# Performance work log

Hardware: AMD Instinct MI355X
Metric: run time of the kernel (lower is better)

The kernel has to match this reference:

```python
import jax, jax.numpy as jnp
import numpy as np

N = 100000      # nodes
E = 1200000     # edges (avg degree 12)
DIN = 64        # input_dim
HID = 64        # hidden_dim
HEADS = 4
CH = HID // 4   # 16 per-head channels; concat -> HID


def setup_inputs() -> dict:
    key = jax.random.key(0)
    ks = jax.random.split(key, 16)
    s = 0.05
    return {
        "x": jax.random.normal(ks[0], (N, DIN), jnp.float32),
        "edge_index": jax.random.randint(ks[1], (2, E), 0, N, jnp.int32),
        # GCN layers
        "W1": s * jax.random.normal(ks[2], (DIN, HID), jnp.float32),
        "b1": jnp.zeros((HID,), jnp.float32),
        "W2": s * jax.random.normal(ks[3], (HID, HID), jnp.float32),
        "b2": jnp.zeros((HID,), jnp.float32),
        "W3": s * jax.random.normal(ks[4], (HID, HID // 2), jnp.float32),
        "b3": jnp.zeros((HID // 2,), jnp.float32),
        # GAT layer: in = HID//2 = 32, out per head = HID//4 = 16, 4 heads concat -> 64
        "Wg": s * jax.random.normal(ks[5], (HID // 2, HEADS * CH), jnp.float32),
        "att_src": s * jax.random.normal(ks[6], (HEADS, CH), jnp.float32),
        "att_dst": s * jax.random.normal(ks[7], (HEADS, CH), jnp.float32),
        "bg": jnp.zeros((HEADS * CH,), jnp.float32),
        # classifier MLP
        "Wc1": s * jax.random.normal(ks[8], (HID, HID // 2), jnp.float32),
        "bc1": jnp.zeros((HID // 2,), jnp.float32),
        "Wc2": s * jax.random.normal(ks[9], (HID // 2, 2), jnp.float32),
        "bc2": jnp.zeros((2,), jnp.float32),
    }


def reference(x, edge_index, W1, b1, W2, b2, W3, b3,
              Wg, att_src, att_dst, bg, Wc1, bc1, Wc2, bc2):
    n = x.shape[0]
    # add self-loops (PyG default for GCNConv and GATConv)
    loops = jnp.arange(n, dtype=edge_index.dtype)
    src = jnp.concatenate([edge_index[0], loops])
    dst = jnp.concatenate([edge_index[1], loops])

    # symmetric GCN normalization: deg^-1/2[src] * deg^-1/2[dst]
    deg = jax.ops.segment_sum(jnp.ones(src.shape, x.dtype), dst, num_segments=n)
    dinv = jnp.where(deg > 0, jax.lax.rsqrt(deg), 0.0)
    norm = (dinv[src] * dinv[dst])[:, None]  # [E+N, 1]

    def gcn(h, W, b):
        h = h @ W                                   # [N, out]
        msg = h[src] * norm                         # gather + scale, [E+N, out]
        return jax.ops.segment_sum(msg, dst, num_segments=n) + b

    h = jax.nn.relu(gcn(x, W1, b1))   # dropout = identity (eval mode)
    h = jax.nn.relu(gcn(h, W2, b2))
    h = jax.nn.relu(gcn(h, W3, b3))   # [N, HID//2]

    # GATConv, 4 heads, concat
    heads, ch = att_src.shape
    g = (h @ Wg).reshape(n, heads, ch)                       # [N, H, C]
    a_s = jnp.einsum('nhc,hc->nh', g, att_src)               # [N, H]
    a_d = jnp.einsum('nhc,hc->nh', g, att_dst)
    e = jax.nn.leaky_relu(a_s[src] + a_d[dst], 0.2)          # [E+N, H]
    m = jax.ops.segment_max(e, dst, num_segments=n)          # per-dst max
    ex = jnp.exp(e - m[dst])
    den = jax.ops.segment_sum(ex, dst, num_segments=n)
    alpha = ex / den[dst]                                    # segment softmax
    o = jax.ops.segment_sum(g[src] * alpha[:, :, None], dst, num_segments=n)
    o = jax.nn.relu(o.reshape(n, heads * ch) + bg)           # [N, HID]

    pooled = jnp.mean(o, axis=0, keepdims=True)              # batch=None path: [1, HID]
    z = jax.nn.relu(pooled @ Wc1 + bc1)
    return z @ Wc2 + bc2                                     # [1, 2]
```

## Files before the change

kernel.cpp:

```cpp
#include <hip/hip_runtime.h>
#include <hip/hip_bf16.h>
#include <hip/hip_fp16.h>
#include <math.h>

__device__ __forceinline__ unsigned h2u(__half2 h) { return *reinterpret_cast<unsigned*>(&h); }
__device__ __forceinline__ __half2 u2h(unsigned u) { return *reinterpret_cast<__half2*>(&u); }
__device__ __forceinline__ __half2 shfl_h2(__half2 h, int off) {
  int v = __shfl_xor((int)h2u(h), off);
  unsigned uv = (unsigned)v;
  return u2h(uv);
}


#define P1E 16
#define NBK 400

__global__ __launch_bounds__(256) void bucket_hist(const int* __restrict__ dst,
                                                   int* __restrict__ bcnt, int e) {
  __shared__ int lcnt[NBK];
  for (int i = threadIdx.x; i < NBK; i += 256) lcnt[i] = 0;
  __syncthreads();
  int base = blockIdx.x * (256 * P1E);
#pragma unroll
  for (int r = 0; r < P1E; ++r) {
    int i = base + r * 256 + threadIdx.x;
    if (i < e) atomicAdd(&lcnt[dst[i] >> 8], 1);
  }
  __syncthreads();
  for (int b = threadIdx.x; b < NBK; b += 256)
    if (lcnt[b]) atomicAdd(&bcnt[b], lcnt[b]);
}

__global__ __launch_bounds__(512) void bucket_scan(const int* __restrict__ bcnt,
                                                   int* __restrict__ bucket_base,
                                                   int* __restrict__ gcursor,
                                                   int nb, int e) {
  __shared__ int s[512];
  int v = (threadIdx.x < (unsigned)nb) ? bcnt[threadIdx.x] : 0;
  s[threadIdx.x] = v;
  __syncthreads();
  for (int off = 1; off < 512; off <<= 1) {
    int t = (threadIdx.x >= (unsigned)off) ? s[threadIdx.x - off] : 0;
    __syncthreads();
    s[threadIdx.x] += t;
    __syncthreads();
  }
  if (threadIdx.x < (unsigned)nb) {
    int excl = s[threadIdx.x] - v;
    bucket_base[threadIdx.x] = excl;
    gcursor[threadIdx.x] = excl;
  }
  if (threadIdx.x == 0) bucket_base[nb] = e;
}

__global__ __launch_bounds__(256) void bin_pass1(const int* __restrict__ src,
                                                 const int* __restrict__ dst,
                                                 int* __restrict__ gcursor,
                                                 unsigned* __restrict__ stream, int e) {
  __shared__ int lcnt[NBK], gbase[NBK];
  for (int i = threadIdx.x; i < NBK; i += 256) lcnt[i] = 0;
  __syncthreads();
  int base = blockIdx.x * (256 * P1E);
  int rankr[P1E];
#pragma unroll
  for (int r = 0; r < P1E; ++r) {
    int i = base + r * 256 + threadIdx.x;
    rankr[r] = (i < e) ? atomicAdd(&lcnt[dst[i] >> 8], 1) : 0;
  }
  __syncthreads();
  for (int bkt = threadIdx.x; bkt < NBK; bkt += 256)
    gbase[bkt] = lcnt[bkt] ? atomicAdd(&gcursor[bkt], lcnt[bkt]) : 0;
  __syncthreads();
#pragma unroll
  for (int r = 0; r < P1E; ++r) {
    int i = base + r * 256 + threadIdx.x;
    if (i < e) {
      int d = dst[i];
      stream[gbase[d >> 8] + rankr[r]] = ((unsigned)src[i] << 8) | (unsigned)(d & 255);
    }
  }
}


#define LCAP 6144

__global__ __launch_bounds__(256) void bin_pass2(const unsigned* __restrict__ stream,
                                                 const int* __restrict__ bucket_base,
                                                 int* __restrict__ row_start,
                                                 int* __restrict__ cnt,
                                                 int* __restrict__ csr_src,
                                                 int n, int e) {
  __shared__ int lcnt[256];
  __shared__ int lscan[256];
  __shared__ int lcur[256];
  __shared__ int lbuf[LCAP];
  int node_lo = blockIdx.x << 8;
  int nn = min(256, n - node_lo);
  int lo = bucket_base[blockIdx.x];
  int hi = bucket_base[blockIdx.x + 1];
  int sz = hi - lo;
  lcnt[threadIdx.x] = 0;
  __syncthreads();
  for (int j = threadIdx.x; j < sz; j += 256)
    atomicAdd(&lcnt[stream[lo + j] & 255], 1);
  __syncthreads();
  int v = lcnt[threadIdx.x];
  lscan[threadIdx.x] = v;
  __syncthreads();
  for (int off = 1; off < 256; off <<= 1) {
    int t = (threadIdx.x >= (unsigned)off) ? lscan[threadIdx.x - off] : 0;
    __syncthreads();
    lscan[threadIdx.x] += t;
    __syncthreads();
  }
  int excl = lscan[threadIdx.x] - v;
  if ((int)threadIdx.x < nn) {
    row_start[node_lo + threadIdx.x] = lo + excl;
    cnt[node_lo + threadIdx.x] = v;
  }
  if (blockIdx.x == 0 && threadIdx.x == 0) row_start[n] = e;
  lcur[threadIdx.x] = excl;
  __syncthreads();
  if (sz <= LCAP) {
    for (int j = threadIdx.x; j < sz; j += 256) {
      unsigned r = stream[lo + j];
      int slot = atomicAdd(&lcur[r & 255], 1);
      lbuf[slot] = (int)(r >> 8);
    }
    __syncthreads();
    for (int j = threadIdx.x; j < sz; j += 256)
      csr_src[lo + j] = lbuf[j];
  } else {
    for (int j = threadIdx.x; j < sz; j += 256) {
      unsigned r = stream[lo + j];
      int slot = atomicAdd(&lcur[r & 255], 1);
      csr_src[lo + slot] = (int)(r >> 8);
    }
  }
}


template <bool HBF>
__device__ __forceinline__ float4 ld4(const char* rowp, int k) {
  if constexpr (HBF) {
    uint2 v = *reinterpret_cast<const uint2*>(rowp + (size_t)k * 2);
    float2 f01 = __half22float2(u2h(v.x));
    float2 f23 = __half22float2(u2h(v.y));
    float4 r = {f01.x, f01.y, f23.x, f23.y};
    return r;
  } else {
    return *reinterpret_cast<const float4*>(rowp + (size_t)k * 4);
  }
}

#define ACC4(A, HV)                                                              \
  A.x = fmaf(HV.x, w0.x, A.x); A.y = fmaf(HV.x, w0.y, A.y);                      \
  A.z = fmaf(HV.x, w0.z, A.z); A.w = fmaf(HV.x, w0.w, A.w);                      \
  A.x = fmaf(HV.y, w1.x, A.x); A.y = fmaf(HV.y, w1.y, A.y);                      \
  A.z = fmaf(HV.y, w1.z, A.z); A.w = fmaf(HV.y, w1.w, A.w);                      \
  A.x = fmaf(HV.z, w2.x, A.x); A.y = fmaf(HV.z, w2.y, A.y);                      \
  A.z = fmaf(HV.z, w2.z, A.z); A.w = fmaf(HV.z, w2.w, A.w);                      \
  A.x = fmaf(HV.w, w3.x, A.x); A.y = fmaf(HV.w, w3.y, A.y);                      \
  A.z = fmaf(HV.w, w3.z, A.z); A.w = fmaf(HV.w, w3.w, A.w);

template <int IN, int OUT, bool SCALE, bool ATT, bool HBF>
__global__ __launch_bounds__(256) void gemm2x4(const void* __restrict__ Hv,
                                               const float* __restrict__ W,
                                               const int* __restrict__ cnt,
                                               const float* __restrict__ att_src,
                                               const float* __restrict__ att_dst,
                                               unsigned short* __restrict__ T,
                                               float* __restrict__ a_s,
                                               float* __restrict__ a_d, int n) {
  constexpr int TX = OUT / 4;
  constexpr int NB = (256 / TX) * 2;
  constexpr int ESZ = HBF ? 2 : 4;
  __shared__ float Ws[IN * OUT];
  __shared__ float asv[ATT ? OUT : 1], adv[ATT ? OUT : 1];
  __shared__ float lds_as[ATT ? NB * 4 : 1], lds_ad[ATT ? NB * 4 : 1];

  for (int idx = threadIdx.x; idx < IN * OUT / 4; idx += 256)
    reinterpret_cast<float4*>(Ws)[idx] = reinterpret_cast<const float4*>(W)[idx];
  if (ATT) {
    if (threadIdx.x < OUT) {
      asv[threadIdx.x] = att_src[threadIdx.x];
      adv[threadIdx.x] = att_dst[threadIdx.x];
    }
    for (int idx = threadIdx.x; idx < NB * 4; idx += 256) {
      lds_as[idx] = 0.f; lds_ad[idx] = 0.f;
    }
  }
  __syncthreads();

  int tx = threadIdx.x % TX;
  int ty = threadIdx.x / TX;
  int j0 = tx * 4;
  int base = blockIdx.x * NB;
  int n0 = base + ty * 2;

  const char* Hb = (const char*)Hv;
  const char* h0p = Hb + (size_t)min(n0 + 0, n - 1) * IN * ESZ;
  const char* h1p = Hb + (size_t)min(n0 + 1, n - 1) * IN * ESZ;

  float4 acc0 = {0,0,0,0}, acc1 = {0,0,0,0};
#pragma unroll 2
  for (int k = 0; k < IN; k += 4) {
    float4 ha = ld4<HBF>(h0p, k);
    float4 hb = ld4<HBF>(h1p, k);
    float4 w0 = *reinterpret_cast<const float4*>(&Ws[(k + 0) * OUT + j0]);
    float4 w1 = *reinterpret_cast<const float4*>(&Ws[(k + 1) * OUT + j0]);
    float4 w2 = *reinterpret_cast<const float4*>(&Ws[(k + 2) * OUT + j0]);
    float4 w3 = *reinterpret_cast<const float4*>(&Ws[(k + 3) * OUT + j0]);
    ACC4(acc0, ha) ACC4(acc1, hb)
  }

  float4 av[2] = {acc0, acc1};
#pragma unroll
  for (int i = 0; i < 2; ++i) {
    int node = n0 + i;
    if (node < n) {
      float dv = SCALE ? rsqrtf((float)(cnt[node] + 1)) : 1.f;
      float o0 = av[i].x * dv, o1 = av[i].y * dv, o2 = av[i].z * dv, o3 = av[i].w * dv;
      uint2 st;
      st.x = h2u(__floats2half2_rn(o0, o1));
      st.y = h2u(__floats2half2_rn(o2, o3));
      *reinterpret_cast<uint2*>(T + (size_t)node * OUT + j0) = st;
      if (ATT) {
        int head = tx >> 2;
        float cs = o0 * asv[j0] + o1 * asv[j0 + 1] + o2 * asv[j0 + 2] + o3 * asv[j0 + 3];
        float cd = o0 * adv[j0] + o1 * adv[j0 + 1] + o2 * adv[j0 + 2] + o3 * adv[j0 + 3];
        atomicAdd(&lds_as[(ty * 2 + i) * 4 + head], cs);
        atomicAdd(&lds_ad[(ty * 2 + i) * 4 + head], cd);
      }
    }
  }
  if (ATT) {
    __syncthreads();
    for (int idx = threadIdx.x; idx < NB * 4; idx += 256) {
      int node = base + (idx >> 2);
      if (node < n) {
        a_s[(size_t)base * 4 + idx] = lds_as[idx];
        a_d[(size_t)base * 4 + idx] = lds_ad[idx];
      }
    }
  }
}


template <int C>
__global__ __launch_bounds__(256) void gcn_agg(const unsigned short* __restrict__ T,
                                               const int* __restrict__ row_start,
                                               const int* __restrict__ csr_src,
                                               const int* __restrict__ cnt,
                                               const float* __restrict__ b,
                                               unsigned short* __restrict__ out, int n) {
  constexpr int LPR = C / 8;
  constexpr int SLOTS = 64 / LPR;
  constexpr unsigned RS4 = C / 8;
  int wid = threadIdx.x >> 6;
  int lane = threadIdx.x & 63;
  int node = blockIdx.x * 4 + wid;
  if (node >= n) return;
  int q = lane & (LPR - 1);
  int g = lane / LPR;
  const uint4* Tp = reinterpret_cast<const uint4*>(T);
  int rs = row_start[node], re = row_start[node + 1];
  __half2 A0 = u2h(0u), A1 = u2h(0u), A2 = u2h(0u), A3 = u2h(0u);
  if (g == 0) {
    uint4 v = Tp[(unsigned)node * RS4 + q];
    A0 = u2h(v.x); A1 = u2h(v.y); A2 = u2h(v.z); A3 = u2h(v.w);
  }
  if constexpr (C == 64) {
    __half2 B0 = u2h(0u), B1 = u2h(0u), B2 = u2h(0u), B3 = u2h(0u);
    int i = rs + g;
    while (i < re) {
      bool v2 = (i + 8) < re;
      unsigned s1 = (unsigned)csr_src[i];
      unsigned s2 = v2 ? (unsigned)csr_src[i + 8] : s1;
      uint4 r1 = Tp[s1 * RS4 + q];
      uint4 r2 = Tp[s2 * RS4 + q];
      if (!v2) { r2.x = 0u; r2.y = 0u; r2.z = 0u; r2.w = 0u; }
      A0 = __hadd2(A0, u2h(r1.x)); A1 = __hadd2(A1, u2h(r1.y));
      A2 = __hadd2(A2, u2h(r1.z)); A3 = __hadd2(A3, u2h(r1.w));
      B0 = __hadd2(B0, u2h(r2.x)); B1 = __hadd2(B1, u2h(r2.y));
      B2 = __hadd2(B2, u2h(r2.z)); B3 = __hadd2(B3, u2h(r2.w));
      i += 16;
    }
    A0 = __hadd2(A0, B0); A1 = __hadd2(A1, B1);
    A2 = __hadd2(A2, B2); A3 = __hadd2(A3, B3);
  } else {
    for (int i = rs + g; i < re; i += SLOTS) {
      unsigned s = (unsigned)csr_src[i];
      uint4 v = Tp[s * RS4 + q];
      A0 = __hadd2(A0, u2h(v.x)); A1 = __hadd2(A1, u2h(v.y));
      A2 = __hadd2(A2, u2h(v.z)); A3 = __hadd2(A3, u2h(v.w));
    }
  }
#pragma unroll
  for (int off = LPR; off < 64; off <<= 1) {
    A0 = __hadd2(A0, shfl_h2(A0, off));
    A1 = __hadd2(A1, shfl_h2(A1, off));
    A2 = __hadd2(A2, shfl_h2(A2, off));
    A3 = __hadd2(A3, shfl_h2(A3, off));
  }
  if (lane < LPR) {
    float dn = rsqrtf((float)(cnt[node] + 1));
    float4 b0 = *reinterpret_cast<const float4*>(b + 8 * q);
    float4 b1 = *reinterpret_cast<const float4*>(b + 8 * q + 4);
    float2 f0 = __half22float2(A0), f1 = __half22float2(A1);
    float2 f2 = __half22float2(A2), f3 = __half22float2(A3);
    uint4 o;
    o.x = h2u(__floats2half2_rn(fmaxf(fmaf(dn, f0.x, b0.x), 0.f),
                                fmaxf(fmaf(dn, f0.y, b0.y), 0.f)));
    o.y = h2u(__floats2half2_rn(fmaxf(fmaf(dn, f1.x, b0.z), 0.f),
                                fmaxf(fmaf(dn, f1.y, b0.w), 0.f)));
    o.z = h2u(__floats2half2_rn(fmaxf(fmaf(dn, f2.x, b1.x), 0.f),
                                fmaxf(fmaf(dn, f2.y, b1.y), 0.f)));
    o.w = h2u(__floats2half2_rn(fmaxf(fmaf(dn, f3.x, b1.z), 0.f),
                                fmaxf(fmaf(dn, f3.y, b1.w), 0.f)));
    reinterpret_cast<uint4*>(out)[(unsigned)node * RS4 + q] = o;
  }
}


__device__ __forceinline__ float lrelu(float v) { return v > 0.f ? v : 0.2f * v; }

__global__ __launch_bounds__(256) void gat_agg(const unsigned short* __restrict__ g,
                                               const float* __restrict__ a_s,
                                               const float* __restrict__ a_d,
                                               const int* __restrict__ row_start,
                                               const int* __restrict__ csr_src,
                                               const float* __restrict__ bg,
                                               unsigned short* __restrict__ out, int n) {
  int wid = threadIdx.x >> 6;
  int lane = threadIdx.x & 63;
  int node = blockIdx.x * 4 + wid;
  if (node >= n) return;
  int q = lane & 7;
  int gslot = lane >> 3;
  int h = q >> 1;
  const uint4* gp = reinterpret_cast<const uint4*>(g);
  int rs = row_start[node], re = row_start[node + 1];
  float ad_h = a_d[(unsigned)node * 4u + h];
  float den = 0.f, den2 = 0.f;
  __half2 A0 = u2h(0u), A1 = u2h(0u), A2 = u2h(0u), A3 = u2h(0u);
  __half2 C0 = u2h(0u), C1 = u2h(0u), C2 = u2h(0u), C3 = u2h(0u);
  if (gslot == 0) {
    float w = __expf(lrelu(a_s[(unsigned)node * 4u + h] + ad_h));
    uint4 v = gp[(unsigned)node * 8u + q];
    den = w;
    __half2 w2 = __float2half2_rn(w);
    A0 = __hmul2(w2, u2h(v.x)); A1 = __hmul2(w2, u2h(v.y));
    A2 = __hmul2(w2, u2h(v.z)); A3 = __hmul2(w2, u2h(v.w));
  }
  int i = rs + gslot;
  while (i < re) {
    bool v2 = (i + 8) < re;
    unsigned s1 = (unsigned)csr_src[i];
    unsigned s2 = v2 ? (unsigned)csr_src[i + 8] : s1;
    float e1 = a_s[s1 * 4u + h];
    float e2 = a_s[s2 * 4u + h];
    uint4 r1 = gp[s1 * 8u + q];
    uint4 r2 = gp[s2 * 8u + q];
    float w1 = __expf(lrelu(e1 + ad_h));
    float w2 = v2 ? __expf(lrelu(e2 + ad_h)) : 0.f;
    den += w1;
    den2 += w2;
    __half2 hw1 = __float2half2_rn(w1);
    __half2 hw2 = __float2half2_rn(w2);
    A0 = __hfma2(hw1, u2h(r1.x), A0); A1 = __hfma2(hw1, u2h(r1.y), A1);
    A2 = __hfma2(hw1, u2h(r1.z), A2); A3 = __hfma2(hw1, u2h(r1.w), A3);
    C0 = __hfma2(hw2, u2h(r2.x), C0); C1 = __hfma2(hw2, u2h(r2.y), C1);
    C2 = __hfma2(hw2, u2h(r2.z), C2); C3 = __hfma2(hw2, u2h(r2.w), C3);
    i += 16;
  }
  den += den2;
  A0 = __hadd2(A0, C0); A1 = __hadd2(A1, C1);
  A2 = __hadd2(A2, C2); A3 = __hadd2(A3, C3);
#pragma unroll
  for (int off = 8; off < 64; off <<= 1) {
    den += __shfl_xor(den, off);
    A0 = __hadd2(A0, shfl_h2(A0, off));
    A1 = __hadd2(A1, shfl_h2(A1, off));
    A2 = __hadd2(A2, shfl_h2(A2, off));
    A3 = __hadd2(A3, shfl_h2(A3, off));
  }
  if (lane < 8) {
    float inv = 1.f / den;
    float4 b0 = *reinterpret_cast<const float4*>(bg + 8 * q);
    float4 b1 = *reinterpret_cast<const float4*>(bg + 8 * q + 4);
    float2 f0 = __half22float2(A0), f1 = __half22float2(A1);
    float2 f2 = __half22float2(A2), f3 = __half22float2(A3);
    uint4 o;
    o.x = h2u(__floats2half2_rn(fmaxf(fmaf(f0.x, inv, b0.x), 0.f),
                                fmaxf(fmaf(f0.y, inv, b0.y), 0.f)));
    o.y = h2u(__floats2half2_rn(fmaxf(fmaf(f1.x, inv, b0.z), 0.f),
                                fmaxf(fmaf(f1.y, inv, b0.w), 0.f)));
    o.z = h2u(__floats2half2_rn(fmaxf(fmaf(f2.x, inv, b1.x), 0.f),
                                fmaxf(fmaf(f2.y, inv, b1.y), 0.f)));
    o.w = h2u(__floats2half2_rn(fmaxf(fmaf(f3.x, inv, b1.z), 0.f),
                                fmaxf(fmaf(f3.y, inv, b1.w), 0.f)));
    reinterpret_cast<uint4*>(out)[(unsigned)node * 8u + q] = o;
  }
}


#define PBLK 512

__global__ __launch_bounds__(256) void pool_partial(const unsigned short* __restrict__ O,
                                                    double* __restrict__ partial, int n) {
  const unsigned* Op = reinterpret_cast<const unsigned*>(O);
  unsigned total = (unsigned)n * 32u;
  unsigned tid = blockIdx.x * 256u + threadIdx.x;
  unsigned stride = PBLK * 256u;
  double a0 = 0.0, a1 = 0.0;
  for (unsigned i = tid; i < total; i += stride) {
    float2 f = __half22float2(u2h(Op[i]));
    a0 += (double)f.x;
    a1 += (double)f.y;
  }
  __shared__ double red0[256], red1[256];
  red0[threadIdx.x] = a0;
  red1[threadIdx.x] = a1;
  __syncthreads();
  int t = threadIdx.x;
  if (t < 32) {
    double s0 = 0.0, s1 = 0.0;
#pragma unroll
    for (int k = 0; k < 8; ++k) {
      s0 += red0[t + 32 * k];
      s1 += red1[t + 32 * k];
    }
    partial[(size_t)blockIdx.x * 64 + 2 * t]     = s0;
    partial[(size_t)blockIdx.x * 64 + 2 * t + 1] = s1;
  }
}

__global__ __launch_bounds__(64) void final_kernel(const double* __restrict__ partial, int nblocks,
                                                   const float* __restrict__ Wc1,
                                                   const float* __restrict__ bc1,
                                                   const float* __restrict__ Wc2,
                                                   const float* __restrict__ bc2,
                                                   float* __restrict__ out, int n) {
  __shared__ float pooled[64];
  __shared__ float z[32];
  int t = threadIdx.x;
  double s = 0.0;
#pragma unroll 4
  for (int b = 0; b < nblocks; ++b) s += partial[(size_t)b * 64 + t];
  pooled[t] = (float)(s / (double)n);
  __syncthreads();
  if (t < 32) {
    double a = 0.0;
    for (int k = 0; k < 64; ++k) a += (double)pooled[k] * (double)Wc1[k * 32 + t];
    z[t] = fmaxf((float)a + bc1[t], 0.f);
  }
  __syncthreads();
  if (t < 2) {
    double a = 0.0;
    for (int j = 0; j < 32; ++j) a += (double)z[j] * (double)Wc2[j * 2 + t];
    out[t] = (float)a + bc2[t];
  }
}


extern "C" void kernel_launch(void* const* d_in, const int* in_sizes, int n_in,
                              void* d_out, int out_size, void* d_ws, size_t ws_size,
                              hipStream_t stream) {
  const float* x   = (const float*)d_in[0];
  const int* eidx  = (const int*)d_in[1];
  const float* W1  = (const float*)d_in[2];
  const float* b1  = (const float*)d_in[3];
  const float* W2  = (const float*)d_in[4];
  const float* b2  = (const float*)d_in[5];
  const float* W3  = (const float*)d_in[6];
  const float* b3  = (const float*)d_in[7];
  const float* Wg  = (const float*)d_in[8];
  const float* att_src = (const float*)d_in[9];
  const float* att_dst = (const float*)d_in[10];
  const float* bg  = (const float*)d_in[11];
  const float* Wc1 = (const float*)d_in[12];
  const float* bc1 = (const float*)d_in[13];
  const float* Wc2 = (const float*)d_in[14];
  const float* bc2 = (const float*)d_in[15];

  const int n = in_sizes[0] / 64;
  const int e = in_sizes[1] / 2;
  const int* src = eidx;
  const int* dst = eidx + e;

  char* ws = (char*)d_ws;
  size_t off = 0;
  auto alloc = [&](size_t bytes) {
    void* p = ws + off;
    off += (bytes + 255) & ~(size_t)255;
    return p;
  };
  const int nbuckets = (n + 255) >> 8;
  int*      cnt        = (int*)alloc((size_t)n * 4);
  int*      row_start  = (int*)alloc(((size_t)n + 1) * 4);
  unsigned* stream_b   = (unsigned*)alloc((size_t)e * 4);
  int*      csr_src    = (int*)alloc((size_t)e * 4);
  int*      bcnt       = (int*)alloc(NBK * 4);
  int*      bucket_base = (int*)alloc((NBK + 1) * 4);
  int*      gcursor    = (int*)alloc(NBK * 4);
  unsigned short* bufT = (unsigned short*)alloc((size_t)n * 64 * 2);
  unsigned short* bufF = (unsigned short*)alloc((size_t)n * 64 * 2);
  float*    a_s        = (float*)alloc((size_t)n * 4 * 4);
  float*    a_d        = (float*)alloc((size_t)n * 4 * 4);
  double*   partial    = (double*)alloc((size_t)PBLK * 64 * 8);

  hipMemsetAsync(bcnt, 0, NBK * 4, stream);

  int nblk4 = (n + 3) / 4;
  int g64 = (n + 31) / 32;
  int g32 = (n + 63) / 64;
  int p1blk = (e + 256 * P1E - 1) / (256 * P1E);

  bucket_hist<<<p1blk, 256, 0, stream>>>(dst, bcnt, e);
  bucket_scan<<<1, 512, 0, stream>>>(bcnt, bucket_base, gcursor, nbuckets, e);
  bin_pass1<<<p1blk, 256, 0, stream>>>(src, dst, gcursor, stream_b, e);
  bin_pass2<<<nbuckets, 256, 0, stream>>>(stream_b, bucket_base, row_start, cnt,
                                          csr_src, n, e);

  gemm2x4<64, 64, true, false, false><<<g64, 256, 0, stream>>>(x, W1, cnt, nullptr, nullptr,
                                                               bufT, nullptr, nullptr, n);
  gcn_agg<64><<<nblk4, 256, 0, stream>>>(bufT, row_start, csr_src, cnt, b1, bufF, n);
  gemm2x4<64, 64, true, false, true><<<g64, 256, 0, stream>>>(bufF, W2, cnt, nullptr, nullptr,
                                                              bufT, nullptr, nullptr, n);
  gcn_agg<64><<<nblk4, 256, 0, stream>>>(bufT, row_start, csr_src, cnt, b2, bufF, n);
  gemm2x4<64, 32, true, false, true><<<g32, 256, 0, stream>>>(bufF, W3, cnt, nullptr, nullptr,
                                                              bufT, nullptr, nullptr, n);
  gcn_agg<32><<<nblk4, 256, 0, stream>>>(bufT, row_start, csr_src, cnt, b3, bufF, n);
  gemm2x4<32, 64, false, true, true><<<g64, 256, 0, stream>>>(bufF, Wg, nullptr, att_src, att_dst,
                                                              bufT, a_s, a_d, n);
  gat_agg<<<nblk4, 256, 0, stream>>>(bufT, a_s, a_d, row_start, csr_src, bg, bufF, n);
  pool_partial<<<PBLK, 256, 0, stream>>>(bufF, partial, n);
  final_kernel<<<1, 64, 0, stream>>>(partial, PBLK, Wc1, bc1, Wc2, bc2, (float*)d_out, n);
}
```

Measured before the change: 323.2 us.

## Overlap first GEMM with histogram, move dinv scaling into aggregation, fuse GAT pooling

The first X@W1 GEMM now runs in the same launch as the bucket histogram, because it does not depend on the CSR build. The source-side degree normalization is moved out of the GEMMs: layer 1 applies it per edge in the aggregation, and later layers pre-scale the outputs of the previous aggregation. The GAT aggregation writes per-block column partial sums for the mean pool instead of the full node features, so the pooling pass reads far less data. In exchange, layer 1 does an extra gather of cnt per edge with half-precision weighting, and the extra scaling may change rounding.

```diff
diff --git a/kernel.cpp b/kernel.cpp
--- a/kernel.cpp
+++ b/kernel.cpp
@@ -15,20 +15,70 @@
 #define P1E 16
 #define NBK 400
 
-__global__ __launch_bounds__(256) void bucket_hist(const int* __restrict__ dst,
-                                                   int* __restrict__ bcnt, int e) {
+__global__ __launch_bounds__(256) void hist_gemm1(const int* __restrict__ dst,
+                                                  int* __restrict__ bcnt, int e,
+                                                  int fillBlocks,
+                                                  const float* __restrict__ H,
+                                                  const float* __restrict__ W,
+                                                  unsigned short* __restrict__ T, int n) {
   __shared__ int lcnt[NBK];
-  for (int i = threadIdx.x; i < NBK; i += 256) lcnt[i] = 0;
-  __syncthreads();
-  int base = blockIdx.x * (256 * P1E);
-#pragma unroll
-  for (int r = 0; r < P1E; ++r) {
-    int i = base + r * 256 + threadIdx.x;
-    if (i < e) atomicAdd(&lcnt[dst[i] >> 8], 1);
-  }
-  __syncthreads();
-  for (int b = threadIdx.x; b < NBK; b += 256)
-    if (lcnt[b]) atomicAdd(&bcnt[b], lcnt[b]);
+  __shared__ float Ws[64 * 64];
+  if ((int)blockIdx.x < fillBlocks) {
+    for (int i = threadIdx.x; i < NBK; i += 256) lcnt[i] = 0;
+    __syncthreads();
+    int base = blockIdx.x * (256 * P1E);
+#pragma unroll
+    for (int r = 0; r < P1E; ++r) {
+      int i = base + r * 256 + threadIdx.x;
+      if (i < e) atomicAdd(&lcnt[dst[i] >> 8], 1);
+    }
+    __syncthreads();
+    for (int b = threadIdx.x; b < NBK; b += 256)
+      if (lcnt[b]) atomicAdd(&bcnt[b], lcnt[b]);
+    return;
+  }
+  for (int idx = threadIdx.x; idx < 64 * 64 / 4; idx += 256)
+    reinterpret_cast<float4*>(Ws)[idx] = reinterpret_cast<const float4*>(W)[idx];
+  __syncthreads();
+  int bid = blockIdx.x - fillBlocks;
+  int tx = threadIdx.x % 16;
+  int ty = threadIdx.x / 16;
+  int j0 = tx * 4;
+  int n0 = bid * 32 + ty * 2;
+  const float* h0p = H + (size_t)min(n0 + 0, n - 1) * 64;
+  const float* h1p = H + (size_t)min(n0 + 1, n - 1) * 64;
+  float4 acc0 = {0,0,0,0}, acc1 = {0,0,0,0};
+#pragma unroll 2
+  for (int k = 0; k < 64; k += 4) {
+    float4 ha = *reinterpret_cast<const float4*>(h0p + k);
+    float4 hb = *reinterpret_cast<const float4*>(h1p + k);
+    float4 w0 = *reinterpret_cast<const float4*>(&Ws[(k + 0) * 64 + j0]);
+    float4 w1 = *reinterpret_cast<const float4*>(&Ws[(k + 1) * 64 + j0]);
+    float4 w2 = *reinterpret_cast<const float4*>(&Ws[(k + 2) * 64 + j0]);
+    float4 w3 = *reinterpret_cast<const float4*>(&Ws[(k + 3) * 64 + j0]);
+#define A4(A, HV)                                                                \
+    A.x = fmaf(HV.x, w0.x, A.x); A.y = fmaf(HV.x, w0.y, A.y);                    \
+    A.z = fmaf(HV.x, w0.z, A.z); A.w = fmaf(HV.x, w0.w, A.w);                    \
+    A.x = fmaf(HV.y, w1.x, A.x); A.y = fmaf(HV.y, w1.y, A.y);                    \
+    A.z = fmaf(HV.y, w1.z, A.z); A.w = fmaf(HV.y, w1.w, A.w);                    \
+    A.x = fmaf(HV.z, w2.x, A.x); A.y = fmaf(HV.z, w2.y, A.y);                    \
+    A.z = fmaf(HV.z, w2.z, A.z); A.w = fmaf(HV.z, w2.w, A.w);                    \
+    A.x = fmaf(HV.w, w3.x, A.x); A.y = fmaf(HV.w, w3.y, A.y);                    \
+    A.z = fmaf(HV.w, w3.z, A.z); A.w = fmaf(HV.w, w3.w, A.w);
+    A4(acc0, ha) A4(acc1, hb)
+#undef A4
+  }
+  float4 av[2] = {acc0, acc1};
+#pragma unroll
+  for (int i = 0; i < 2; ++i) {
+    int node = n0 + i;
+    if (node < n) {
+      uint2 st;
+      st.x = h2u(__floats2half2_rn(av[i].x, av[i].y));
+      st.y = h2u(__floats2half2_rn(av[i].z, av[i].w));
+      *reinterpret_cast<uint2*>(T + (size_t)node * 64 + j0) = st;
+    }
+  }
 }
 
 __global__ __launch_bounds__(512) void bucket_scan(const int* __restrict__ bcnt,
@@ -140,33 +190,9 @@
 }
 
 
-template <bool HBF>
-__device__ __forceinline__ float4 ld4(const char* rowp, int k) {
-  if constexpr (HBF) {
-    uint2 v = *reinterpret_cast<const uint2*>(rowp + (size_t)k * 2);
-    float2 f01 = __half22float2(u2h(v.x));
-    float2 f23 = __half22float2(u2h(v.y));
-    float4 r = {f01.x, f01.y, f23.x, f23.y};
-    return r;
-  } else {
-    return *reinterpret_cast<const float4*>(rowp + (size_t)k * 4);
-  }
-}
-
-#define ACC4(A, HV)                                                              \
-  A.x = fmaf(HV.x, w0.x, A.x); A.y = fmaf(HV.x, w0.y, A.y);                      \
-  A.z = fmaf(HV.x, w0.z, A.z); A.w = fmaf(HV.x, w0.w, A.w);                      \
-  A.x = fmaf(HV.y, w1.x, A.x); A.y = fmaf(HV.y, w1.y, A.y);                      \
-  A.z = fmaf(HV.y, w1.z, A.z); A.w = fmaf(HV.y, w1.w, A.w);                      \
-  A.x = fmaf(HV.z, w2.x, A.x); A.y = fmaf(HV.z, w2.y, A.y);                      \
-  A.z = fmaf(HV.z, w2.z, A.z); A.w = fmaf(HV.z, w2.w, A.w);                      \
-  A.x = fmaf(HV.w, w3.x, A.x); A.y = fmaf(HV.w, w3.y, A.y);                      \
-  A.z = fmaf(HV.w, w3.z, A.z); A.w = fmaf(HV.w, w3.w, A.w);
-
-template <int IN, int OUT, bool SCALE, bool ATT, bool HBF>
-__global__ __launch_bounds__(256) void gemm2x4(const void* __restrict__ Hv,
+template <int IN, int OUT, bool ATT>
+__global__ __launch_bounds__(256) void gemm2x4(const unsigned short* __restrict__ Hh,
                                                const float* __restrict__ W,
-                                               const int* __restrict__ cnt,
                                                const float* __restrict__ att_src,
                                                const float* __restrict__ att_dst,
                                                unsigned short* __restrict__ T,
@@ -174,7 +200,6 @@
                                                float* __restrict__ a_d, int n) {
   constexpr int TX = OUT / 4;
   constexpr int NB = (256 / TX) * 2;
-  constexpr int ESZ = HBF ? 2 : 4;
   __shared__ float Ws[IN * OUT];
   __shared__ float asv[ATT ? OUT : 1], adv[ATT ? OUT : 1];
   __shared__ float lds_as[ATT ? NB * 4 : 1], lds_ad[ATT ? NB * 4 : 1];
@@ -198,20 +223,33 @@
   int base = blockIdx.x * NB;
   int n0 = base + ty * 2;
 
-  const char* Hb = (const char*)Hv;
-  const char* h0p = Hb + (size_t)min(n0 + 0, n - 1) * IN * ESZ;
-  const char* h1p = Hb + (size_t)min(n0 + 1, n - 1) * IN * ESZ;
+  const unsigned short* h0p = Hh + (size_t)min(n0 + 0, n - 1) * IN;
+  const unsigned short* h1p = Hh + (size_t)min(n0 + 1, n - 1) * IN;
 
   float4 acc0 = {0,0,0,0}, acc1 = {0,0,0,0};
 #pragma unroll 2
   for (int k = 0; k < IN; k += 4) {
-    float4 ha = ld4<HBF>(h0p, k);
-    float4 hb = ld4<HBF>(h1p, k);
+    uint2 va = *reinterpret_cast<const uint2*>(h0p + k);
+    uint2 vb = *reinterpret_cast<const uint2*>(h1p + k);
+    float2 a01 = __half22float2(u2h(va.x)), a23 = __half22float2(u2h(va.y));
+    float2 b01 = __half22float2(u2h(vb.x)), b23 = __half22float2(u2h(vb.y));
+    float4 ha = {a01.x, a01.y, a23.x, a23.y};
+    float4 hb = {b01.x, b01.y, b23.x, b23.y};
     float4 w0 = *reinterpret_cast<const float4*>(&Ws[(k + 0) * OUT + j0]);
     float4 w1 = *reinterpret_cast<const float4*>(&Ws[(k + 1) * OUT + j0]);
     float4 w2 = *reinterpret_cast<const float4*>(&Ws[(k + 2) * OUT + j0]);
     float4 w3 = *reinterpret_cast<const float4*>(&Ws[(k + 3) * OUT + j0]);
-    ACC4(acc0, ha) ACC4(acc1, hb)
+#define A4(A, HV)                                                                \
+    A.x = fmaf(HV.x, w0.x, A.x); A.y = fmaf(HV.x, w0.y, A.y);                    \
+    A.z = fmaf(HV.x, w0.z, A.z); A.w = fmaf(HV.x, w0.w, A.w);                    \
+    A.x = fmaf(HV.y, w1.x, A.x); A.y = fmaf(HV.y, w1.y, A.y);                    \
+    A.z = fmaf(HV.y, w1.z, A.z); A.w = fmaf(HV.y, w1.w, A.w);                    \
+    A.x = fmaf(HV.z, w2.x, A.x); A.y = fmaf(HV.z, w2.y, A.y);                    \
+    A.z = fmaf(HV.z, w2.z, A.z); A.w = fmaf(HV.z, w2.w, A.w);                    \
+    A.x = fmaf(HV.w, w3.x, A.x); A.y = fmaf(HV.w, w3.y, A.y);                    \
+    A.z = fmaf(HV.w, w3.z, A.z); A.w = fmaf(HV.w, w3.w, A.w);
+    A4(acc0, ha) A4(acc1, hb)
+#undef A4
   }
 
   float4 av[2] = {acc0, acc1};
@@ -219,8 +257,7 @@
   for (int i = 0; i < 2; ++i) {
     int node = n0 + i;
     if (node < n) {
-      float dv = SCALE ? rsqrtf((float)(cnt[node] + 1)) : 1.f;
-      float o0 = av[i].x * dv, o1 = av[i].y * dv, o2 = av[i].z * dv, o3 = av[i].w * dv;
+      float o0 = av[i].x, o1 = av[i].y, o2 = av[i].z, o3 = av[i].w;
       uint2 st;
       st.x = h2u(__floats2half2_rn(o0, o1));
       st.y = h2u(__floats2half2_rn(o2, o3));
@@ -247,7 +284,7 @@
 }
 
 
-template <int C>
+template <int C, bool DINV, bool PRE>
 __global__ __launch_bounds__(256) void gcn_agg(const unsigned short* __restrict__ T,
                                                const int* __restrict__ row_start,
                                                const int* __restrict__ csr_src,
@@ -265,10 +302,17 @@
   int g = lane / LPR;
   const uint4* Tp = reinterpret_cast<const uint4*>(T);
   int rs = row_start[node], re = row_start[node + 1];
+  float dn = rsqrtf((float)(cnt[node] + 1));
   __half2 A0 = u2h(0u), A1 = u2h(0u), A2 = u2h(0u), A3 = u2h(0u);
   if (g == 0) {
     uint4 v = Tp[(unsigned)node * RS4 + q];
-    A0 = u2h(v.x); A1 = u2h(v.y); A2 = u2h(v.z); A3 = u2h(v.w);
+    if constexpr (DINV) {
+      __half2 hw = __float2half2_rn(dn);
+      A0 = __hmul2(hw, u2h(v.x)); A1 = __hmul2(hw, u2h(v.y));
+      A2 = __hmul2(hw, u2h(v.z)); A3 = __hmul2(hw, u2h(v.w));
+    } else {
+      A0 = u2h(v.x); A1 = u2h(v.y); A2 = u2h(v.z); A3 = u2h(v.w);
+    }
   }
   if constexpr (C == 64) {
     __half2 B0 = u2h(0u), B1 = u2h(0u), B2 = u2h(0u), B3 = u2h(0u);
@@ -279,11 +323,22 @@
       unsigned s2 = v2 ? (unsigned)csr_src[i + 8] : s1;
       uint4 r1 = Tp[s1 * RS4 + q];
       uint4 r2 = Tp[s2 * RS4 + q];
-      if (!v2) { r2.x = 0u; r2.y = 0u; r2.z = 0u; r2.w = 0u; }
-      A0 = __hadd2(A0, u2h(r1.x)); A1 = __hadd2(A1, u2h(r1.y));
-      A2 = __hadd2(A2, u2h(r1.z)); A3 = __hadd2(A3, u2h(r1.w));
-      B0 = __hadd2(B0, u2h(r2.x)); B1 = __hadd2(B1, u2h(r2.y));
-      B2 = __hadd2(B2, u2h(r2.z)); B3 = __hadd2(B3, u2h(r2.w));
+      if constexpr (DINV) {
+        float w1f = rsqrtf((float)(cnt[s1] + 1));
+        float w2f = v2 ? rsqrtf((float)(cnt[s2] + 1)) : 0.f;
+        __half2 hw1 = __float2half2_rn(w1f);
+        __half2 hw2 = __float2half2_rn(w2f);
+        A0 = __hfma2(hw1, u2h(r1.x), A0); A1 = __hfma2(hw1, u2h(r1.y), A1);
+        A2 = __hfma2(hw1, u2h(r1.z), A2); A3 = __hfma2(hw1, u2h(r1.w), A3);
+        B0 = __hfma2(hw2, u2h(r2.x), B0); B1 = __hfma2(hw2, u2h(r2.y), B1);
+        B2 = __hfma2(hw2, u2h(r2.z), B2); B3 = __hfma2(hw2, u2h(r2.w), B3);
+      } else {
+        if (!v2) { r2.x = 0u; r2.y = 0u; r2.z = 0u; r2.w = 0u; }
+        A0 = __hadd2(A0, u2h(r1.x)); A1 = __hadd2(A1, u2h(r1.y));
+        A2 = __hadd2(A2, u2h(r1.z)); A3 = __hadd2(A3, u2h(r1.w));
+        B0 = __hadd2(B0, u2h(r2.x)); B1 = __hadd2(B1, u2h(r2.y));
+        B2 = __hadd2(B2, u2h(r2.z)); B3 = __hadd2(B3, u2h(r2.w));
+      }
       i += 16;
     }
     A0 = __hadd2(A0, B0); A1 = __hadd2(A1, B1);
@@ -304,20 +359,24 @@
     A3 = __hadd2(A3, shfl_h2(A3, off));
   }
   if (lane < LPR) {
-    float dn = rsqrtf((float)(cnt[node] + 1));
     float4 b0 = *reinterpret_cast<const float4*>(b + 8 * q);
     float4 b1 = *reinterpret_cast<const float4*>(b + 8 * q + 4);
     float2 f0 = __half22float2(A0), f1 = __half22float2(A1);
     float2 f2 = __half22float2(A2), f3 = __half22float2(A3);
+    float sc = PRE ? dn : 1.f;
+    float r0 = sc * fmaxf(fmaf(dn, f0.x, b0.x), 0.f);
+    float r1 = sc * fmaxf(fmaf(dn, f0.y, b0.y), 0.f);
+    float r2 = sc * fmaxf(fmaf(dn, f1.x, b0.z), 0.f);
+    float r3 = sc * fmaxf(fmaf(dn, f1.y, b0.w), 0.f);
+    float r4 = sc * fmaxf(fmaf(dn, f2.x, b1.x), 0.f);
+    float r5 = sc * fmaxf(fmaf(dn, f2.y, b1.y), 0.f);
+    float r6 = sc * fmaxf(fmaf(dn, f3.x, b1.z), 0.f);
+    float r7 = sc * fmaxf(fmaf(dn, f3.y, b1.w), 0.f);
     uint4 o;
-    o.x = h2u(__floats2half2_rn(fmaxf(fmaf(dn, f0.x, b0.x), 0.f),
-                                fmaxf(fmaf(dn, f0.y, b0.y), 0.f)));
-    o.y = h2u(__floats2half2_rn(fmaxf(fmaf(dn, f1.x, b0.z), 0.f),
-                                fmaxf(fmaf(dn, f1.y, b0.w), 0.f)));
-    o.z = h2u(__floats2half2_rn(fmaxf(fmaf(dn, f2.x, b1.x), 0.f),
-                                fmaxf(fmaf(dn, f2.y, b1.y), 0.f)));
-    o.w = h2u(__floats2half2_rn(fmaxf(fmaf(dn, f3.x, b1.z), 0.f),
-                                fmaxf(fmaf(dn, f3.y, b1.w), 0.f)));
+    o.x = h2u(__floats2half2_rn(r0, r1));
+    o.y = h2u(__floats2half2_rn(r2, r3));
+    o.z = h2u(__floats2half2_rn(r4, r5));
+    o.w = h2u(__floats2half2_rn(r6, r7));
     reinterpret_cast<uint4*>(out)[(unsigned)node * RS4 + q] = o;
   }
 }
@@ -331,21 +390,27 @@
                                                const int* __restrict__ row_start,
                                                const int* __restrict__ csr_src,
                                                const float* __restrict__ bg,
-                                               unsigned short* __restrict__ out, int n) {
+                                               float* __restrict__ partial1, int n) {
+  __shared__ float pacc[4][64];
   int wid = threadIdx.x >> 6;
   int lane = threadIdx.x & 63;
   int node = blockIdx.x * 4 + wid;
-  if (node >= n) return;
+  bool active = node < n;
   int q = lane & 7;
   int gslot = lane >> 3;
   int h = q >> 1;
   const uint4* gp = reinterpret_cast<const uint4*>(g);
-  int rs = row_start[node], re = row_start[node + 1];
-  float ad_h = a_d[(unsigned)node * 4u + h];
+  int rs = 0, re = 0;
+  float ad_h = 0.f;
+  if (active) {
+    rs = row_start[node];
+    re = row_start[node + 1];
+    ad_h = a_d[(unsigned)node * 4u + h];
+  }
   float den = 0.f, den2 = 0.f;
   __half2 A0 = u2h(0u), A1 = u2h(0u), A2 = u2h(0u), A3 = u2h(0u);
   __half2 C0 = u2h(0u), C1 = u2h(0u), C2 = u2h(0u), C3 = u2h(0u);
-  if (gslot == 0) {
+  if (active && gslot == 0) {
     float w = __expf(lrelu(a_s[(unsigned)node * 4u + h] + ad_h));
     uint4 v = gp[(unsigned)node * 8u + q];
     den = w;
@@ -386,53 +451,46 @@
     A3 = __hadd2(A3, shfl_h2(A3, off));
   }
   if (lane < 8) {
-    float inv = 1.f / den;
+    float inv = active ? (1.f / den) : 0.f;
     float4 b0 = *reinterpret_cast<const float4*>(bg + 8 * q);
     float4 b1 = *reinterpret_cast<const float4*>(bg + 8 * q + 4);
     float2 f0 = __half22float2(A0), f1 = __half22float2(A1);
     float2 f2 = __half22float2(A2), f3 = __half22float2(A3);
-    uint4 o;
-    o.x = h2u(__floats2half2_rn(fmaxf(fmaf(f0.x, inv, b0.x), 0.f),
-                                fmaxf(fmaf(f0.y, inv, b0.y), 0.f)));
-    o.y = h2u(__floats2half2_rn(fmaxf(fmaf(f1.x, inv, b0.z), 0.f),
-                                fmaxf(fmaf(f1.y, inv, b0.w), 0.f)));
-    o.z = h2u(__floats2half2_rn(fmaxf(fmaf(f2.x, inv, b1.x), 0.f),
-                                fmaxf(fmaf(f2.y, inv, b1.y), 0.f)));
-    o.w = h2u(__floats2half2_rn(fmaxf(fmaf(f3.x, inv, b1.z), 0.f),
-                                fmaxf(fmaf(f3.y, inv, b1.w), 0.f)));
-    reinterpret_cast<uint4*>(out)[(unsigned)node * 8u + q] = o;
+    int c0 = 8 * q;
+    pacc[wid][c0 + 0] = active ? fmaxf(fmaf(f0.x, inv, b0.x), 0.f) : 0.f;
+    pacc[wid][c0 + 1] = active ? fmaxf(fmaf(f0.y, inv, b0.y), 0.f) : 0.f;
+    pacc[wid][c0 + 2] = active ? fmaxf(fmaf(f1.x, inv, b0.z), 0.f) : 0.f;
+    pacc[wid][c0 + 3] = active ? fmaxf(fmaf(f1.y, inv, b0.w), 0.f) : 0.f;
+    pacc[wid][c0 + 4] = active ? fmaxf(fmaf(f2.x, inv, b1.x), 0.f) : 0.f;
+    pacc[wid][c0 + 5] = active ? fmaxf(fmaf(f2.y, inv, b1.y), 0.f) : 0.f;
+    pacc[wid][c0 + 6] = active ? fmaxf(fmaf(f3.x, inv, b1.z), 0.f) : 0.f;
+    pacc[wid][c0 + 7] = active ? fmaxf(fmaf(f3.y, inv, b1.w), 0.f) : 0.f;
+  }
+  __syncthreads();
+  if (threadIdx.x < 64) {
+    int t = threadIdx.x;
+    partial1[(size_t)blockIdx.x * 64 + t] =
+        pacc[0][t] + pacc[1][t] + pacc[2][t] + pacc[3][t];
   }
 }
 
 
 #define PBLK 512
 
-__global__ __launch_bounds__(256) void pool_partial(const unsigned short* __restrict__ O,
-                                                    double* __restrict__ partial, int n) {
-  const unsigned* Op = reinterpret_cast<const unsigned*>(O);
-  unsigned total = (unsigned)n * 32u;
+__global__ __launch_bounds__(256) void pool_partial(const float* __restrict__ P1,
+                                                    double* __restrict__ partial2,
+                                                    unsigned total) {
   unsigned tid = blockIdx.x * 256u + threadIdx.x;
   unsigned stride = PBLK * 256u;
-  double a0 = 0.0, a1 = 0.0;
-  for (unsigned i = tid; i < total; i += stride) {
-    float2 f = __half22float2(u2h(Op[i]));
-    a0 += (double)f.x;
-    a1 += (double)f.y;
-  }
-  __shared__ double red0[256], red1[256];
-  red0[threadIdx.x] = a0;
-  red1[threadIdx.x] = a1;
-  __syncthreads();
-  int t = threadIdx.x;
-  if (t < 32) {
-    double s0 = 0.0, s1 = 0.0;
-#pragma unroll
-    for (int k = 0; k < 8; ++k) {
-      s0 += red0[t + 32 * k];
-      s1 += red1[t + 32 * k];
-    }
-    partial[(size_t)blockIdx.x * 64 + 2 * t]     = s0;
-    partial[(size_t)blockIdx.x * 64 + 2 * t + 1] = s1;
+  double a = 0.0;
+  for (unsigned i = tid; i < total; i += stride) a += (double)P1[i];
+  __shared__ double red[256];
+  red[threadIdx.x] = a;
+  __syncthreads();
+  if (threadIdx.x < 64) {
+    int t = threadIdx.x;
+    double s = red[t] + red[t + 64] + red[t + 128] + red[t + 192];
+    partial2[(size_t)blockIdx.x * 64 + t] = s;
   }
 }
 
@@ -497,6 +555,7 @@
     return p;
   };
   const int nbuckets = (n + 255) >> 8;
+  const int nblk4 = (n + 3) / 4;
   int*      cnt        = (int*)alloc((size_t)n * 4);
   int*      row_start  = (int*)alloc(((size_t)n + 1) * 4);
   unsigned* stream_b   = (unsigned*)alloc((size_t)e * 4);
@@ -508,33 +567,31 @@
   unsigned short* bufF = (unsigned short*)alloc((size_t)n * 64 * 2);
   float*    a_s        = (float*)alloc((size_t)n * 4 * 4);
   float*    a_d        = (float*)alloc((size_t)n * 4 * 4);
-  double*   partial    = (double*)alloc((size_t)PBLK * 64 * 8);
+  float*    partial1   = (float*)alloc((size_t)nblk4 * 64 * 4);
+  double*   partial2   = (double*)alloc((size_t)PBLK * 64 * 8);
 
   hipMemsetAsync(bcnt, 0, NBK * 4, stream);
 
-  int nblk4 = (n + 3) / 4;
   int g64 = (n + 31) / 32;
   int g32 = (n + 63) / 64;
   int p1blk = (e + 256 * P1E - 1) / (256 * P1E);
 
-  bucket_hist<<<p1blk, 256, 0, stream>>>(dst, bcnt, e);
+  hist_gemm1<<<p1blk + g64, 256, 0, stream>>>(dst, bcnt, e, p1blk, x, W1, bufT, n);
   bucket_scan<<<1, 512, 0, stream>>>(bcnt, bucket_base, gcursor, nbuckets, e);
   bin_pass1<<<p1blk, 256, 0, stream>>>(src, dst, gcursor, stream_b, e);
   bin_pass2<<<nbuckets, 256, 0, stream>>>(stream_b, bucket_base, row_start, cnt,
                                           csr_src, n, e);
 
-  gemm2x4<64, 64, true, false, false><<<g64, 256, 0, stream>>>(x, W1, cnt, nullptr, nullptr,
-                                                               bufT, nullptr, nullptr, n);
-  gcn_agg<64><<<nblk4, 256, 0, stream>>>(bufT, row_start, csr_src, cnt, b1, bufF, n);
-  gemm2x4<64, 64, true, false, true><<<g64, 256, 0, stream>>>(bufF, W2, cnt, nullptr, nullptr,
-                                                              bufT, nullptr, nullptr, n);
-  gcn_agg<64><<<nblk4, 256, 0, stream>>>(bufT, row_start, csr_src, cnt, b2, bufF, n);
-  gemm2x4<64, 32, true, false, true><<<g32, 256, 0, stream>>>(bufF, W3, cnt, nullptr, nullptr,
-                                                              bufT, nullptr, nullptr, n);
-  gcn_agg<32><<<nblk4, 256, 0, stream>>>(bufT, row_start, csr_src, cnt, b3, bufF, n);
-  gemm2x4<32, 64, false, true, true><<<g64, 256, 0, stream>>>(bufF, Wg, nullptr, att_src, att_dst,
-                                                              bufT, a_s, a_d, n);
-  gat_agg<<<nblk4, 256, 0, stream>>>(bufT, a_s, a_d, row_start, csr_src, bg, bufF, n);
-  pool_partial<<<PBLK, 256, 0, stream>>>(bufF, partial, n);
-  final_kernel<<<1, 64, 0, stream>>>(partial, PBLK, Wc1, bc1, Wc2, bc2, (float*)d_out, n);
-}
+  gcn_agg<64, true, true><<<nblk4, 256, 0, stream>>>(bufT, row_start, csr_src, cnt, b1, bufF, n);
+  gemm2x4<64, 64, false><<<g64, 256, 0, stream>>>(bufF, W2, nullptr, nullptr,
+                                                  bufT, nullptr, nullptr, n);
+  gcn_agg<64, false, true><<<nblk4, 256, 0, stream>>>(bufT, row_start, csr_src, cnt, b2, bufF, n);
+  gemm2x4<64, 32, false><<<g32, 256, 0, stream>>>(bufF, W3, nullptr, nullptr,
+                                                  bufT, nullptr, nullptr, n);
+  gcn_agg<32, false, false><<<nblk4, 256, 0, stream>>>(bufT, row_start, csr_src, cnt, b3, bufF, n);
+  gemm2x4<32, 64, true><<<g64, 256, 0, stream>>>(bufF, Wg, att_src, att_dst,
+                                                 bufT, a_s, a_d, n);
+  gat_agg<<<nblk4, 256, 0, stream>>>(bufT, a_s, a_d, row_start, csr_src, bg, partial1, n);
+  pool_partial<<<PBLK, 256, 0, stream>>>(partial1, partial2, (unsigned)nblk4 * 64u);
+  final_kernel<<<1, 64, 0, stream>>>(partial2, PBLK, Wc1, bc1, Wc2, bc2, (float*)d_out, n);
+}
```

After: 315.6 us. 2.4% less time.
